# Kernel optimization log

Measured on AMD Instinct MI355X. Metric: run time of the kernel, lower is better.

The kernel has to match this reference:

```python
import jax, jax.numpy as jnp
import numpy as np

BS, S, H, KVH, HD = 4, 4096, 32, 8, 128
BLK = 32                      # tokens per cache page
NB = S // BLK                 # blocks per sequence (128)
NPAGES = BS * NB              # total pages in pool (512)
WIN = 1024                    # sliding window
G = H // KVH                  # query heads per KV head (GQA group)
SCALE = 1.0 / float(np.sqrt(HD))
NEG = -1e30


def setup_inputs() -> dict:
    key = jax.random.key(0)
    k0, k1, k2, k3 = jax.random.split(key, 4)
    q = jax.random.normal(k0, (BS, S, H, HD), dtype=jnp.float32)
    k = jax.random.normal(k1, (BS, S, KVH, HD), dtype=jnp.float32)
    v = jax.random.normal(k2, (BS, S, KVH, HD), dtype=jnp.float32)
    k_cache = jnp.zeros((NPAGES, BLK, KVH, HD), dtype=jnp.float32)
    v_cache = jnp.zeros((NPAGES, BLK, KVH, HD), dtype=jnp.float32)
    # identity block table: page p holds block (p % NB) of sequence (p // NB)
    seq_block_ids = jnp.arange(NPAGES, dtype=jnp.int32).reshape(BS, NB)
    start_positions = jnp.full((BS,), S - 1, dtype=jnp.int32)  # decode last token
    mask = jnp.zeros((BS, 1, 1, S), dtype=jnp.float32)         # additive mask
    sink = jax.random.normal(k3, (H,), dtype=jnp.float32)      # per-head sink logit
    return {"q": q, "k": k, "v": v, "k_cache": k_cache, "v_cache": v_cache,
            "mask": mask, "sink": sink, "seq_block_ids": seq_block_ids,
            "start_positions": start_positions}


def reference(q, k, v, k_cache, v_cache, mask, sink, seq_block_ids, start_positions):
    # ---- prefill: write full k/v into the paged cache ----
    # (the wrapper discards the prefill attention output; cache write is its
    #  only observable effect on the returned decode output)
    kp = k.reshape(BS, NB, BLK, KVH, HD)
    vp = v.reshape(BS, NB, BLK, KVH, HD)
    k_cache = k_cache.at[seq_block_ids].set(kp)
    v_cache = v_cache.at[seq_block_ids].set(vp)

    # ---- decode: write last-token k/v at start_positions ----
    b = jnp.arange(BS)
    pages = seq_block_ids[b, start_positions // BLK]   # [BS]
    offs = start_positions % BLK                       # [BS]
    k_cache = k_cache.at[pages, offs].set(k[:, -1])
    v_cache = v_cache.at[pages, offs].set(v[:, -1])

    # ---- gather cache back into dense [BS, S, KVH, HD] via block table ----
    k_all = k_cache[seq_block_ids].reshape(BS, S, KVH, HD)
    v_all = v_cache[seq_block_ids].reshape(BS, S, KVH, HD)

    # ---- last-token paged attention with sliding window + sink ----
    q_last = q[:, -1].reshape(BS, KVH, G, HD)          # group query heads by KV head
    scores = jnp.einsum('bhgd,bjhd->bhgj', q_last, k_all) * SCALE  # [BS,KVH,G,S]
    scores = scores + mask                              # mask broadcasts over heads
    pos = jnp.arange(S, dtype=jnp.int32)
    p = start_positions[:, None]
    valid = (pos[None, :] <= p) & (p - pos[None, :] < WIN)          # [BS,S]
    scores = jnp.where(valid[:, None, None, :], scores, NEG)

    # softmax with an extra per-head sink logit that contributes no value
    sink_l = sink.reshape(KVH, G)[None, :, :, None]     # [1,KVH,G,1]
    m = jnp.maximum(jnp.max(scores, axis=-1, keepdims=True), sink_l)
    e = jnp.exp(scores - m)
    denom = jnp.sum(e, axis=-1, keepdims=True) + jnp.exp(sink_l - m)
    attn = e / denom                                    # [BS,KVH,G,S]

    out = jnp.einsum('bhgj,bjhd->bhgd', attn, v_all)    # [BS,KVH,G,HD]
    return out.reshape(BS, 1, H, HD)
```

## Files before the change

kernel.cpp:

```cpp
#include <hip/hip_runtime.h>
#include <math.h>

#define BS 4
#define S 4096
#define H 32
#define KVH 8
#define HD 128
#define G 4
#define WIN 1024
#define SCALE 0.08838834764831843f

#define NSPLIT 32
#define CHUNK (WIN / NSPLIT)
#define PSTRIDE 132

#define GLOAD_LDS16(gsrc, ldst) \
    __builtin_amdgcn_global_load_lds( \
        (const __attribute__((address_space(1))) void*)(gsrc), \
        (__attribute__((address_space(3))) void*)(ldst), 16, 0, 0)

template <int CTRL>
__device__ __forceinline__ float dpp_mov(float x) {
    return __int_as_float(__builtin_amdgcn_update_dpp(
        0, __float_as_int(x), CTRL, 0xF, 0xF, true));
}
__device__ __forceinline__ float red_add16(float d) {
    d += dpp_mov<0xB1>(d);
    d += dpp_mov<0x4E>(d);
    d += dpp_mov<0x124>(d);
    d += dpp_mov<0x128>(d);
    return d;
}
__device__ __forceinline__ float red_max16(float d) {
    d = fmaxf(d, dpp_mov<0xB1>(d));
    d = fmaxf(d, dpp_mov<0x4E>(d));
    d = fmaxf(d, dpp_mov<0x124>(d));
    d = fmaxf(d, dpp_mov<0x128>(d));
    return d;
}

__global__ __launch_bounds__(256) void attn_split_kernel(
    const float* __restrict__ q, const float* __restrict__ k,
    const float* __restrict__ v, const float* __restrict__ mask,
    const int* __restrict__ start_positions, float* __restrict__ ws)
{
    const int blk   = blockIdx.x;
    const int split = blk % NSPLIT;
    const int kvh   = (blk / NSPLIT) % KVH;
    const int b     = blk / (NSPLIT * KVH);
    const int tid   = threadIdx.x;
    const int g     = tid >> 6;
    const int lane  = tid & 63;
    const int grp   = lane >> 4;
    const int l16   = lane & 15;
    const int h     = kvh * G + g;

    const int p = start_positions[b];
    const int base_pos = p - WIN + 1 + split * CHUNK;

    __shared__ float kbuf[CHUNK][HD];
    __shared__ float vbuf[CHUNK][HD];
    __shared__ float sc[G][CHUNK];

    const size_t kv_base = (size_t)b * S * (KVH * HD) + (size_t)kvh * HD;

    {
        const int srow = lane >> 5;
        const int scol = (lane & 31) * 4;
        #pragma unroll
        for (int i = 0; i < 4; ++i) {
            const int st  = g * 4 + i;
            const int r   = st * 2 + srow;
            const int pos = base_pos + r;
            const int row = (pos == p) ? (S - 1) : (pos < 0 ? 0 : pos);
            const float* ksrc = k + kv_base + (size_t)row * (KVH * HD) + scol;
            const float* vsrc = v + kv_base + (size_t)row * (KVH * HD) + scol;
            GLOAD_LDS16(ksrc, (char*)&kbuf[0][0] + st * 1024);
            GLOAD_LDS16(vsrc, (char*)&vbuf[0][0] + st * 1024);
        }
    }

    const int lpos = base_pos + (lane & 31);
    const float msk = (lpos >= 0) ? mask[(size_t)b * S + lpos] : 0.f;

    const float* qptr = q + (((size_t)b * S + (S - 1)) * H + h) * HD + l16 * 8;
    const float4 qa = *(const float4*)(qptr);
    const float4 qb = *(const float4*)(qptr + 4);

    __syncthreads();

    #pragma unroll
    for (int it = 0; it < CHUNK / 4; ++it) {
        const int jj = it * 4 + grp;
        const float4 ka = *(const float4*)(&kbuf[jj][l16 * 8]);
        const float4 kb = *(const float4*)(&kbuf[jj][l16 * 8 + 4]);
        float d = qa.x * ka.x + qa.y * ka.y + qa.z * ka.z + qa.w * ka.w
                + qb.x * kb.x + qb.y * kb.y + qb.z * kb.z + qb.w * kb.w;
        d = red_add16(d);
        if (l16 == 0) sc[g][jj] = d;
    }

    float s_l = sc[g][lane & (CHUNK - 1)] * SCALE + msk;
    if (lpos < 0) s_l = -1e30f;
    float m = red_max16(s_l);
    m = fmaxf(m, __shfl_xor(m, 16, 64));
    const float e_l = __expf(s_l - m);
    if (lane < CHUNK) sc[g][lane] = e_l;
    float lsum = red_add16(e_l);
    lsum += __shfl_xor(lsum, 16, 64);

    const int half = lane >> 5;
    const int l32  = lane & 31;
    float4 o4 = make_float4(0.f, 0.f, 0.f, 0.f);
    #pragma unroll
    for (int it = 0; it < CHUNK / 2; ++it) {
        const int jj = it * 2 + half;
        const float e = sc[g][jj];
        const float4 v4 = *(const float4*)(&vbuf[jj][l32 * 4]);
        o4.x += e * v4.x; o4.y += e * v4.y; o4.z += e * v4.z; o4.w += e * v4.w;
    }
    o4.x += __shfl_xor(o4.x, 32, 64);
    o4.y += __shfl_xor(o4.y, 32, 64);
    o4.z += __shfl_xor(o4.z, 32, 64);
    o4.w += __shfl_xor(o4.w, 32, 64);

    const size_t widx = ((((size_t)b * KVH + kvh) * G + g) * NSPLIT + split) * (size_t)PSTRIDE;
    if (lane < 32) {
        *(float4*)(ws + widx + 4 * l32) = o4;
        if (lane == 0) { ws[widx + 128] = m; ws[widx + 129] = lsum; }
    }
}

__global__ __launch_bounds__(64) void attn_reduce_kernel(
    const float* __restrict__ ws, const float* __restrict__ sink,
    float* __restrict__ out)
{
    const int blk = blockIdx.x;
    const int h = blk % H;
    const int b = blk / H;
    const int kvh = h / G;
    const int g = h % G;
    const int lane = threadIdx.x;

    const size_t base = ((((size_t)b * KVH + kvh) * G + g) * (size_t)NSPLIT) * (size_t)PSTRIDE;

    const float sk = sink[h];
    float M = sk;
    float ms[NSPLIT];
    #pragma unroll
    for (int s = 0; s < NSPLIT; ++s) {
        ms[s] = ws[base + (size_t)s * PSTRIDE + 128];
        M = fmaxf(M, ms[s]);
    }

    float D = __expf(sk - M);
    float ax = 0.f, ay = 0.f;
    #pragma unroll
    for (int s = 0; s < NSPLIT; ++s) {
        const float w = __expf(ms[s] - M);
        D += w * ws[base + (size_t)s * PSTRIDE + 129];
        const float2 o2 = *(const float2*)(ws + base + (size_t)s * PSTRIDE + 2 * lane);
        ax += w * o2.x;
        ay += w * o2.y;
    }

    const float invD = 1.f / D;
    float2 r; r.x = ax * invD; r.y = ay * invD;
    *(float2*)(out + ((size_t)b * H + h) * HD + 2 * lane) = r;
}

extern "C" void kernel_launch(void* const* d_in, const int* in_sizes, int n_in,
                              void* d_out, int out_size, void* d_ws, size_t ws_size,
                              hipStream_t stream) {
    const float* q    = (const float*)d_in[0];
    const float* k    = (const float*)d_in[1];
    const float* v    = (const float*)d_in[2];
    const float* mask = (const float*)d_in[5];
    const float* sink = (const float*)d_in[6];
    const int* start_positions = (const int*)d_in[8];
    float* out = (float*)d_out;
    float* ws  = (float*)d_ws;

    attn_split_kernel<<<BS * KVH * NSPLIT, 256, 0, stream>>>(q, k, v, mask, start_positions, ws);
    attn_reduce_kernel<<<BS * H, 64, 0, stream>>>(ws, sink, out);
}
```

Baseline: 15.19 us.

## Fuse split-K reduction into attention kernel via last-block atomic counter

Removes the separate reduce kernel launch. Each split block now publishes its partial output with relaxed agent-scope atomics and bumps a per-(batch, kv-head) counter, and the last block to arrive does the cross-split softmax merge using wave shuffles. V loads are also issued after the first barrier so they overlap the QK dot products. A memset of the counters is added before the launch, which costs an extra stream operation. The relaxed ordering between the partial-result stores and the counter increment may be a correctness risk.

```diff
diff --git a/kernel.cpp b/kernel.cpp
--- a/kernel.cpp
+++ b/kernel.cpp
@@ -13,11 +13,15 @@
 #define NSPLIT 32
 #define CHUNK (WIN / NSPLIT)
 #define PSTRIDE 132
+#define WS_PART_OFF 256
 
 #define GLOAD_LDS16(gsrc, ldst) \
     __builtin_amdgcn_global_load_lds( \
         (const __attribute__((address_space(1))) void*)(gsrc), \
         (__attribute__((address_space(3))) void*)(ldst), 16, 0, 0)
+
+#define ASTORE(p, v) __hip_atomic_store((p), (v), __ATOMIC_RELAXED, __HIP_MEMORY_SCOPE_AGENT)
+#define ALOAD(p)     __hip_atomic_load((p), __ATOMIC_RELAXED, __HIP_MEMORY_SCOPE_AGENT)
 
 template <int CTRL>
 __device__ __forceinline__ float dpp_mov(float x) {
@@ -39,10 +43,11 @@
     return d;
 }
 
-__global__ __launch_bounds__(256) void attn_split_kernel(
+__global__ __launch_bounds__(256) void attn_fused_kernel(
     const float* __restrict__ q, const float* __restrict__ k,
     const float* __restrict__ v, const float* __restrict__ mask,
-    const int* __restrict__ start_positions, float* __restrict__ ws)
+    const float* __restrict__ sink, const int* __restrict__ start_positions,
+    float* __restrict__ ws, float* __restrict__ out)
 {
     const int blk   = blockIdx.x;
     const int split = blk % NSPLIT;
@@ -61,23 +66,20 @@
     __shared__ float kbuf[CHUNK][HD];
     __shared__ float vbuf[CHUNK][HD];
     __shared__ float sc[G][CHUNK];
+    __shared__ int last;
 
     const size_t kv_base = (size_t)b * S * (KVH * HD) + (size_t)kvh * HD;
-
-    {
-        const int srow = lane >> 5;
-        const int scol = (lane & 31) * 4;
-        #pragma unroll
-        for (int i = 0; i < 4; ++i) {
-            const int st  = g * 4 + i;
-            const int r   = st * 2 + srow;
-            const int pos = base_pos + r;
-            const int row = (pos == p) ? (S - 1) : (pos < 0 ? 0 : pos);
-            const float* ksrc = k + kv_base + (size_t)row * (KVH * HD) + scol;
-            const float* vsrc = v + kv_base + (size_t)row * (KVH * HD) + scol;
-            GLOAD_LDS16(ksrc, (char*)&kbuf[0][0] + st * 1024);
-            GLOAD_LDS16(vsrc, (char*)&vbuf[0][0] + st * 1024);
-        }
+    const int srow = lane >> 5;
+    const int scol = (lane & 31) * 4;
+
+    #pragma unroll
+    for (int i = 0; i < 4; ++i) {
+        const int st  = g * 4 + i;
+        const int r   = st * 2 + srow;
+        const int pos = base_pos + r;
+        const int row = (pos == p) ? (S - 1) : (pos < 0 ? 0 : pos);
+        GLOAD_LDS16(k + kv_base + (size_t)row * (KVH * HD) + scol,
+                    (char*)&kbuf[0][0] + st * 1024);
     }
 
     const int lpos = base_pos + (lane & 31);
@@ -88,6 +90,16 @@
     const float4 qb = *(const float4*)(qptr + 4);
 
     __syncthreads();
+
+    #pragma unroll
+    for (int i = 0; i < 4; ++i) {
+        const int st  = g * 4 + i;
+        const int r   = st * 2 + srow;
+        const int pos = base_pos + r;
+        const int row = (pos == p) ? (S - 1) : (pos < 0 ? 0 : pos);
+        GLOAD_LDS16(v + kv_base + (size_t)row * (KVH * HD) + scol,
+                    (char*)&vbuf[0][0] + st * 1024);
+    }
 
     #pragma unroll
     for (int it = 0; it < CHUNK / 4; ++it) {
@@ -109,6 +121,8 @@
     float lsum = red_add16(e_l);
     lsum += __shfl_xor(lsum, 16, 64);
 
+    __syncthreads();
+
     const int half = lane >> 5;
     const int l32  = lane & 31;
     float4 o4 = make_float4(0.f, 0.f, 0.f, 0.f);
@@ -124,44 +138,53 @@
     o4.z += __shfl_xor(o4.z, 32, 64);
     o4.w += __shfl_xor(o4.w, 32, 64);
 
-    const size_t widx = ((((size_t)b * KVH + kvh) * G + g) * NSPLIT + split) * (size_t)PSTRIDE;
+    const size_t widx = WS_PART_OFF +
+        ((((size_t)b * KVH + kvh) * G + g) * NSPLIT + split) * (size_t)PSTRIDE;
     if (lane < 32) {
-        *(float4*)(ws + widx + 4 * l32) = o4;
-        if (lane == 0) { ws[widx + 128] = m; ws[widx + 129] = lsum; }
-    }
-}
-
-__global__ __launch_bounds__(64) void attn_reduce_kernel(
-    const float* __restrict__ ws, const float* __restrict__ sink,
-    float* __restrict__ out)
-{
-    const int blk = blockIdx.x;
-    const int h = blk % H;
-    const int b = blk / H;
-    const int kvh = h / G;
-    const int g = h % G;
-    const int lane = threadIdx.x;
-
-    const size_t base = ((((size_t)b * KVH + kvh) * G + g) * (size_t)NSPLIT) * (size_t)PSTRIDE;
-
+        ASTORE(&ws[widx + 4 * l32 + 0], o4.x);
+        ASTORE(&ws[widx + 4 * l32 + 1], o4.y);
+        ASTORE(&ws[widx + 4 * l32 + 2], o4.z);
+        ASTORE(&ws[widx + 4 * l32 + 3], o4.w);
+        if (lane == 0) { ASTORE(&ws[widx + 128], m); ASTORE(&ws[widx + 129], lsum); }
+    }
+
+    asm volatile("s_waitcnt vmcnt(0)" ::: "memory");
+    __syncthreads();
+    if (tid == 0) {
+        int* cnt = (int*)ws + (b * KVH + kvh);
+        last = (__hip_atomic_fetch_add(cnt, 1, __ATOMIC_RELAXED,
+                                       __HIP_MEMORY_SCOPE_AGENT) == NSPLIT - 1);
+    }
+    __syncthreads();
+    if (!last) return;
+
+    const size_t fbase = WS_PART_OFF +
+        ((((size_t)b * KVH + kvh) * G + g) * (size_t)NSPLIT) * (size_t)PSTRIDE;
+
+    float mj = -1e30f, lj = 0.f;
+    if (lane < NSPLIT) {
+        mj = ALOAD(&ws[fbase + (size_t)lane * PSTRIDE + 128]);
+        lj = ALOAD(&ws[fbase + (size_t)lane * PSTRIDE + 129]);
+    }
     const float sk = sink[h];
-    float M = sk;
-    float ms[NSPLIT];
-    #pragma unroll
-    for (int s = 0; s < NSPLIT; ++s) {
-        ms[s] = ws[base + (size_t)s * PSTRIDE + 128];
-        M = fmaxf(M, ms[s]);
-    }
-
-    float D = __expf(sk - M);
+    float M = red_max16(mj);
+    M = fmaxf(M, __shfl_xor(M, 16, 64));
+    M = fmaxf(M, __shfl_xor(M, 32, 64));
+    M = fmaxf(M, sk);
+
+    const float wj = (lane < NSPLIT) ? __expf(mj - M) : 0.f;
+    float D = red_add16(wj * lj);
+    D += __shfl_xor(D, 16, 64);
+    D += __shfl_xor(D, 32, 64);
+    D += __expf(sk - M);
+
     float ax = 0.f, ay = 0.f;
-    #pragma unroll
-    for (int s = 0; s < NSPLIT; ++s) {
-        const float w = __expf(ms[s] - M);
-        D += w * ws[base + (size_t)s * PSTRIDE + 129];
-        const float2 o2 = *(const float2*)(ws + base + (size_t)s * PSTRIDE + 2 * lane);
-        ax += w * o2.x;
-        ay += w * o2.y;
+    #pragma unroll 8
+    for (int i = 0; i < NSPLIT; ++i) {
+        const float wi = __shfl(wj, i, 64);
+        const size_t rec = fbase + (size_t)i * PSTRIDE;
+        ax += wi * ALOAD(&ws[rec + 2 * lane]);
+        ay += wi * ALOAD(&ws[rec + 2 * lane + 1]);
     }
 
     const float invD = 1.f / D;
@@ -181,6 +204,7 @@
     float* out = (float*)d_out;
     float* ws  = (float*)d_ws;
 
-    attn_split_kernel<<<BS * KVH * NSPLIT, 256, 0, stream>>>(q, k, v, mask, start_positions, ws);
-    attn_reduce_kernel<<<BS * H, 64, 0, stream>>>(ws, sink, out);
-}
+    hipMemsetAsync(d_ws, 0, BS * KVH * sizeof(int), stream);
+    attn_fused_kernel<<<BS * KVH * NSPLIT, 256, 0, stream>>>(
+        q, k, v, mask, sink, start_positions, ws, out);
+}
```

Measured after the change: 30.66 us. 2.02x slower.
